# Kernel optimization log

Measured on AMD Instinct MI355X. Metric: run time of the kernel, lower is better.

The kernel has to match this reference:

```python
import jax, jax.numpy as jnp
import numpy as np


def setup_inputs() -> dict:
    key = jax.random.key(0)
    k1, k2 = jax.random.split(key)
    x = jax.random.normal(k1, (4, 2048, 2048), dtype=jnp.float32)
    weight = jax.random.normal(k2, (8192, 2048), dtype=jnp.float32) * 0.02
    return {"x": x, "weight": weight, "bits": 8}


def reference(x, weight, bits):
    # ---- activation quantization (per-row int8-style) ----
    scale = jnp.clip(jnp.max(jnp.abs(x), axis=-1, keepdims=True), 1e-5)  # [..., 1]
    max_val = (1 << (bits - 1)) - 1  # 127 for 8 bits
    x_q = jnp.clip(jnp.round(x * (max_val / scale)), -max_val, max_val)

    # ---- ternary weight quantization (-1, 0, 1) ----
    w_scale = jnp.mean(jnp.abs(weight))
    w_q = jnp.where(weight > 0.5 * w_scale, 1.0, 0.0) + jnp.where(
        weight < -0.5 * w_scale, -1.0, 0.0
    )

    # ---- dequantized linear: (x_q @ (w_q * w_scale)^T) / x_scale ----
    out = jnp.einsum("bsi,oi->bso", x_q, w_q * w_scale) / scale

    # ---- squared ReLU ----
    return jnp.maximum(out, 0.0) ** 2
```

## Files before the change

### kernel.cpp

```cpp
#include <hip/hip_runtime.h>
#include <hip/hip_bf16.h>

typedef __attribute__((ext_vector_type(4))) int i32x4;
typedef __attribute__((ext_vector_type(16))) int i32x16;

#define M_DIM 8192
#define N_DIM 8192
#define K_DIM 2048
#define WCOUNT (N_DIM * K_DIM)


__global__ __launch_bounds__(256) void k_abs_partial(const float* __restrict__ w,
                                                     float* __restrict__ part) {
    int tid = blockIdx.x * 256 + threadIdx.x;
    const float4* w4 = (const float4*)w;
    float s = 0.0f;
    const int total4 = WCOUNT / 4;
    for (int i = tid; i < total4; i += 2048 * 256) {
        float4 v = w4[i];
        s += fabsf(v.x) + fabsf(v.y) + fabsf(v.z) + fabsf(v.w);
    }
    #pragma unroll
    for (int off = 1; off < 64; off <<= 1) s += __shfl_xor(s, off);
    __shared__ float red[4];
    if ((threadIdx.x & 63) == 0) red[threadIdx.x >> 6] = s;
    __syncthreads();
    if (threadIdx.x == 0)
        part[blockIdx.x] = (red[0] + red[1]) + (red[2] + red[3]);
}

__global__ __launch_bounds__(256) void k_abs_final(const float* __restrict__ part,
                                                   float* __restrict__ sum) {
    int t = threadIdx.x;
    float s = 0.0f;
    #pragma unroll
    for (int i = 0; i < 8; i++) s += part[t + i * 256];
    #pragma unroll
    for (int off = 1; off < 64; off <<= 1) s += __shfl_xor(s, off);
    __shared__ float red[4];
    if ((t & 63) == 0) red[t >> 6] = s;
    __syncthreads();
    if (t == 0) sum[0] = (red[0] + red[1]) + (red[2] + red[3]);
}

__global__ __launch_bounds__(256) void k_wquant(const float* __restrict__ w,
                                                const float* __restrict__ sum,
                                                signed char* __restrict__ wqf) {
    const float thr = 0.5f * (sum[0] * (1.0f / 16777216.0f));
    const int g = blockIdx.x * 256 + threadIdx.x;
    const int n = g >> 7;
    const int kc = g & 127;
    const float4* wr = (const float4*)(w + (size_t)n * K_DIM + kc * 16);
    union { signed char c[16]; uint4 v; } pk;
    #pragma unroll
    for (int q = 0; q < 4; q++) {
        float4 v = wr[q];
        pk.c[q * 4 + 0] = v.x > thr ? 1 : (v.x < -thr ? -1 : 0);
        pk.c[q * 4 + 1] = v.y > thr ? 1 : (v.y < -thr ? -1 : 0);
        pk.c[q * 4 + 2] = v.z > thr ? 1 : (v.z < -thr ? -1 : 0);
        pk.c[q * 4 + 3] = v.w > thr ? 1 : (v.w < -thr ? -1 : 0);
    }
    *(uint4*)(wqf + (size_t)(n >> 5) * 65536 + kc * 512 + (n & 31) * 16) = pk.v;
}

__global__ __launch_bounds__(256) void k_xquant(const float* __restrict__ x,
                                                const float* __restrict__ sum,
                                                signed char* __restrict__ xqf,
                                                float* __restrict__ coef) {
    const int row = blockIdx.x;
    const int t = threadIdx.x;
    const float4* xr = (const float4*)(x + (size_t)row * K_DIM);
    float4 a = xr[t * 2];
    float4 b = xr[t * 2 + 1];
    float m = fmaxf(fmaxf(fmaxf(fabsf(a.x), fabsf(a.y)), fmaxf(fabsf(a.z), fabsf(a.w))),
                    fmaxf(fmaxf(fabsf(b.x), fabsf(b.y)), fmaxf(fabsf(b.z), fabsf(b.w))));
    #pragma unroll
    for (int off = 1; off < 64; off <<= 1) m = fmaxf(m, __shfl_xor(m, off));
    __shared__ float red[4];
    if ((t & 63) == 0) red[t >> 6] = m;
    __syncthreads();
    m = fmaxf(fmaxf(red[0], red[1]), fmaxf(red[2], red[3]));
    const float sc = fmaxf(m, 1e-5f);
    if (t == 0) coef[row] = (sum[0] * (1.0f / 16777216.0f)) / sc;
    const float r = 127.0f / sc;
    float q[8] = {a.x, a.y, a.z, a.w, b.x, b.y, b.z, b.w};
    union { signed char c[8]; uint2 v; } pk;
    #pragma unroll
    for (int j = 0; j < 8; j++) {
        float v = rintf(q[j] * r);
        v = fminf(fmaxf(v, -127.0f), 127.0f);
        pk.c[j] = (signed char)v;
    }
    *(uint2*)(xqf + (size_t)(row >> 5) * 65536 + (t >> 1) * 512
              + (row & 31) * 16 + (t & 1) * 8) = pk.v;
}

#define GLDS16(g, l)                                                                   \
    __builtin_amdgcn_global_load_lds((const __attribute__((address_space(1))) void*)(g), \
                                     (__attribute__((address_space(3))) void*)(l), 16, 0, 0)
#define BAR __builtin_amdgcn_s_barrier()
#define VMW(n) asm volatile("s_waitcnt vmcnt(" #n ")" ::: "memory")

__global__ __launch_bounds__(256, 4) void k_gemm(const signed char* __restrict__ xqf,
                                                 const signed char* __restrict__ wqf,
                                                 const float* __restrict__ coef,
                                                 float* __restrict__ out) {
    __shared__ signed char lds[32768];

    const int t = threadIdx.x;
    const int lane = t & 63;
    const int wid = t >> 6;
    const int wm = wid >> 1;
    const int wn = wid & 1;
    const int l31 = lane & 31;
    const int kg = lane >> 5;

    const int bid = blockIdx.x;
    const int xcd = bid & 7;
    const int idx = bid >> 3;
    const int grp = idx >> 5;
    const int w_ = idx & 31;
    const int bcol = grp * 4 + (w_ & 3);
    const int brow = xcd * 8 + ((w_ >> 2) & 7);

    const signed char* aSrc0 = xqf + (size_t)(brow * 4 + (t >> 7)) * 65536 + (t & 127) * 16;
    const signed char* aSrc1 = xqf + (size_t)(brow * 4 + 2 + (t >> 7)) * 65536 + (t & 127) * 16;
    const signed char* bSrc0 = wqf + (size_t)(bcol * 4 + (t >> 7)) * 65536 + (t & 127) * 16;
    const signed char* bSrc1 = wqf + (size_t)(bcol * 4 + 2 + (t >> 7)) * 65536 + (t & 127) * 16;
    const int dst0 = wid * 1024;
    const int dst1 = 4096 + wid * 1024;

#define STG(bufc, kt) do {                                                         \
        GLDS16(aSrc0 + (size_t)(kt) * 2048, lds + (bufc) * 16384 + dst0);          \
        GLDS16(aSrc1 + (size_t)(kt) * 2048, lds + (bufc) * 16384 + dst1);          \
        GLDS16(bSrc0 + (size_t)(kt) * 2048, lds + (bufc) * 16384 + 8192 + dst0);   \
        GLDS16(bSrc1 + (size_t)(kt) * 2048, lds + (bufc) * 16384 + 8192 + dst1);   \
    } while (0)

    const int aRd = wm * 4096 + lane * 16;
    const int bRd = 8192 + wn * 4096 + lane * 16;

    i32x16 acc00 = (i32x16){0,0,0,0,0,0,0,0,0,0,0,0,0,0,0,0};
    i32x16 acc01 = acc00, acc10 = acc00, acc11 = acc00;

#define MMK(bufc) do {                                                             \
        const int ab = (bufc) * 16384 + aRd;                                       \
        const int bb = (bufc) * 16384 + bRd;                                       \
        i32x4 a00 = *(const i32x4*)&lds[ab];                                       \
        i32x4 a10 = *(const i32x4*)&lds[ab + 2048];                                \
        i32x4 b00 = *(const i32x4*)&lds[bb];                                       \
        i32x4 b10 = *(const i32x4*)&lds[bb + 2048];                                \
        i32x4 a01 = *(const i32x4*)&lds[ab + 1024];                                \
        i32x4 a11 = *(const i32x4*)&lds[ab + 3072];                                \
        i32x4 b01 = *(const i32x4*)&lds[bb + 1024];                                \
        i32x4 b11 = *(const i32x4*)&lds[bb + 3072];                                \
        __builtin_amdgcn_s_setprio(1);                                             \
        acc00 = __builtin_amdgcn_mfma_i32_32x32x32_i8(a00, b00, acc00, 0, 0, 0);   \
        acc01 = __builtin_amdgcn_mfma_i32_32x32x32_i8(a00, b10, acc01, 0, 0, 0);   \
        acc10 = __builtin_amdgcn_mfma_i32_32x32x32_i8(a10, b00, acc10, 0, 0, 0);   \
        acc11 = __builtin_amdgcn_mfma_i32_32x32x32_i8(a10, b10, acc11, 0, 0, 0);   \
        acc00 = __builtin_amdgcn_mfma_i32_32x32x32_i8(a01, b01, acc00, 0, 0, 0);   \
        acc01 = __builtin_amdgcn_mfma_i32_32x32x32_i8(a01, b11, acc01, 0, 0, 0);   \
        acc10 = __builtin_amdgcn_mfma_i32_32x32x32_i8(a11, b01, acc10, 0, 0, 0);   \
        acc11 = __builtin_amdgcn_mfma_i32_32x32x32_i8(a11, b11, acc11, 0, 0, 0);   \
        __builtin_amdgcn_s_setprio(0); } while (0)

    STG(0, 0);
    STG(1, 1);
    VMW(4);
    BAR;

    #pragma unroll 1
    for (int j = 0; j < 15; j++) {
        const int kt = 2 * j;
        MMK(0); BAR;
        STG(0, kt + 2); VMW(4);
        BAR;
        MMK(1); BAR;
        STG(1, kt + 3); VMW(4);
        BAR;
    }
    MMK(0); BAR;
    VMW(0);
    BAR;
    MMK(1);

    const int rb = brow * 128 + wm * 64 + 4 * kg;
    const int cb = bcol * 128 + wn * 64 + l31;
    #pragma unroll
    for (int mt = 0; mt < 2; mt++) {
        const i32x16 ac0 = mt ? acc10 : acc00;
        const i32x16 ac1 = mt ? acc11 : acc01;
        #pragma unroll
        for (int r = 0; r < 16; r++) {
            const int grow = rb + mt * 32 + (r & 3) + 8 * (r >> 2);
            const float c = coef[grow];
            float v0 = (float)ac0[r] * c; v0 = fmaxf(v0, 0.0f);
            float v1 = (float)ac1[r] * c; v1 = fmaxf(v1, 0.0f);
            __builtin_nontemporal_store(v0 * v0, &out[(size_t)grow * N_DIM + cb]);
            __builtin_nontemporal_store(v1 * v1, &out[(size_t)grow * N_DIM + cb + 32]);
        }
    }
#undef STG
#undef MMK
}

extern "C" void kernel_launch(void* const* d_in, const int* in_sizes, int n_in,
                              void* d_out, int out_size, void* d_ws, size_t ws_size,
                              hipStream_t stream) {
    const float* x = (const float*)d_in[0];
    const float* w = (const float*)d_in[1];
    float* out = (float*)d_out;

    char* ws = (char*)d_ws;
    float* sum   = (float*)ws;
    float* part  = (float*)(ws + 256);
    float* coef  = (float*)(ws + 49152);
    signed char* xqf = (signed char*)(ws + 131072);
    signed char* wqf = (signed char*)(ws + 131072 + 16777216);

    k_abs_partial<<<2048, 256, 0, stream>>>(w, part);
    k_abs_final<<<1, 256, 0, stream>>>(part, sum);
    k_wquant<<<4096, 256, 0, stream>>>(w, sum, wqf);
    k_xquant<<<M_DIM, 256, 0, stream>>>(x, sum, xqf, coef);
    k_gemm<<<dim3(4096), 256, 0, stream>>>(xqf, wqf, coef, out);
}
```

Before: 194.4 us.

## Drop LDS staging in int8 GEMM and load MFMA fragments directly from global

The GEMM stops staging A/B tiles through LDS with global_load_lds and barriers. Each wave now loads its MFMA fragments straight from the pre-swizzled global buffers into registers, double-buffered in registers (fx/fy), and occupancy is lowered to 3 blocks per SM. This removes LDS traffic and barrier sync. The cost is that tiles shared between waves (each A tile is used by two waves, likewise each B tile) are fetched twice from L2/global, and register pressure goes up.

```diff
diff --git a/kernel.cpp b/kernel.cpp
--- a/kernel.cpp
+++ b/kernel.cpp
@@ -95,18 +95,10 @@
               + (row & 31) * 16 + (t & 1) * 8) = pk.v;
 }
 
-#define GLDS16(g, l)                                                                   \
-    __builtin_amdgcn_global_load_lds((const __attribute__((address_space(1))) void*)(g), \
-                                     (__attribute__((address_space(3))) void*)(l), 16, 0, 0)
-#define BAR __builtin_amdgcn_s_barrier()
-#define VMW(n) asm volatile("s_waitcnt vmcnt(" #n ")" ::: "memory")
-
-__global__ __launch_bounds__(256, 4) void k_gemm(const signed char* __restrict__ xqf,
+__global__ __launch_bounds__(256, 3) void k_gemm(const signed char* __restrict__ xqf,
                                                  const signed char* __restrict__ wqf,
                                                  const float* __restrict__ coef,
                                                  float* __restrict__ out) {
-    __shared__ signed char lds[32768];
-
     const int t = threadIdx.x;
     const int lane = t & 63;
     const int wid = t >> 6;
@@ -123,74 +115,55 @@
     const int bcol = grp * 4 + (w_ & 3);
     const int brow = xcd * 8 + ((w_ >> 2) & 7);
 
-    const signed char* aSrc0 = xqf + (size_t)(brow * 4 + (t >> 7)) * 65536 + (t & 127) * 16;
-    const signed char* aSrc1 = xqf + (size_t)(brow * 4 + 2 + (t >> 7)) * 65536 + (t & 127) * 16;
-    const signed char* bSrc0 = wqf + (size_t)(bcol * 4 + (t >> 7)) * 65536 + (t & 127) * 16;
-    const signed char* bSrc1 = wqf + (size_t)(bcol * 4 + 2 + (t >> 7)) * 65536 + (t & 127) * 16;
-    const int dst0 = wid * 1024;
-    const int dst1 = 4096 + wid * 1024;
-
-#define STG(bufc, kt) do {                                                         \
-        GLDS16(aSrc0 + (size_t)(kt) * 2048, lds + (bufc) * 16384 + dst0);          \
-        GLDS16(aSrc1 + (size_t)(kt) * 2048, lds + (bufc) * 16384 + dst1);          \
-        GLDS16(bSrc0 + (size_t)(kt) * 2048, lds + (bufc) * 16384 + 8192 + dst0);   \
-        GLDS16(bSrc1 + (size_t)(kt) * 2048, lds + (bufc) * 16384 + 8192 + dst1);   \
-    } while (0)
-
-    const int aRd = wm * 4096 + lane * 16;
-    const int bRd = 8192 + wn * 4096 + lane * 16;
-
-    i32x16 acc00 = (i32x16){0,0,0,0,0,0,0,0,0,0,0,0,0,0,0,0};
-    i32x16 acc01 = acc00, acc10 = acc00, acc11 = acc00;
-
-#define MMK(bufc) do {                                                             \
-        const int ab = (bufc) * 16384 + aRd;                                       \
-        const int bb = (bufc) * 16384 + bRd;                                       \
-        i32x4 a00 = *(const i32x4*)&lds[ab];                                       \
-        i32x4 a10 = *(const i32x4*)&lds[ab + 2048];                                \
-        i32x4 b00 = *(const i32x4*)&lds[bb];                                       \
-        i32x4 b10 = *(const i32x4*)&lds[bb + 2048];                                \
-        i32x4 a01 = *(const i32x4*)&lds[ab + 1024];                                \
-        i32x4 a11 = *(const i32x4*)&lds[ab + 3072];                                \
-        i32x4 b01 = *(const i32x4*)&lds[bb + 1024];                                \
-        i32x4 b11 = *(const i32x4*)&lds[bb + 3072];                                \
+    const signed char* pa0 = xqf + (size_t)(brow * 4 + wm * 2) * 65536 + lane * 16;
+    const signed char* pa1 = pa0 + 65536;
+    const signed char* pb0 = wqf + (size_t)(bcol * 4 + wn * 2) * 65536 + lane * 16;
+    const signed char* pb1 = pb0 + 65536;
+
+    i32x16 c00 = (i32x16){0,0,0,0,0,0,0,0,0,0,0,0,0,0,0,0};
+    i32x16 c01 = c00, c10 = c00, c11 = c00;
+    i32x4 fx[8], fy[8];
+
+#define LOADF(F, o) do {                                                           \
+        F[0] = *(const i32x4*)(pa0 + (o));                                         \
+        F[1] = *(const i32x4*)(pa0 + (o) + 1024);                                  \
+        F[2] = *(const i32x4*)(pa1 + (o));                                         \
+        F[3] = *(const i32x4*)(pa1 + (o) + 1024);                                  \
+        F[4] = *(const i32x4*)(pb0 + (o));                                         \
+        F[5] = *(const i32x4*)(pb0 + (o) + 1024);                                  \
+        F[6] = *(const i32x4*)(pb1 + (o));                                         \
+        F[7] = *(const i32x4*)(pb1 + (o) + 1024); } while (0)
+#define MMF(F) do {                                                                \
         __builtin_amdgcn_s_setprio(1);                                             \
-        acc00 = __builtin_amdgcn_mfma_i32_32x32x32_i8(a00, b00, acc00, 0, 0, 0);   \
-        acc01 = __builtin_amdgcn_mfma_i32_32x32x32_i8(a00, b10, acc01, 0, 0, 0);   \
-        acc10 = __builtin_amdgcn_mfma_i32_32x32x32_i8(a10, b00, acc10, 0, 0, 0);   \
-        acc11 = __builtin_amdgcn_mfma_i32_32x32x32_i8(a10, b10, acc11, 0, 0, 0);   \
-        acc00 = __builtin_amdgcn_mfma_i32_32x32x32_i8(a01, b01, acc00, 0, 0, 0);   \
-        acc01 = __builtin_amdgcn_mfma_i32_32x32x32_i8(a01, b11, acc01, 0, 0, 0);   \
-        acc10 = __builtin_amdgcn_mfma_i32_32x32x32_i8(a11, b01, acc10, 0, 0, 0);   \
-        acc11 = __builtin_amdgcn_mfma_i32_32x32x32_i8(a11, b11, acc11, 0, 0, 0);   \
+        c00 = __builtin_amdgcn_mfma_i32_32x32x32_i8(F[0], F[4], c00, 0, 0, 0);     \
+        c01 = __builtin_amdgcn_mfma_i32_32x32x32_i8(F[0], F[6], c01, 0, 0, 0);     \
+        c10 = __builtin_amdgcn_mfma_i32_32x32x32_i8(F[2], F[4], c10, 0, 0, 0);     \
+        c11 = __builtin_amdgcn_mfma_i32_32x32x32_i8(F[2], F[6], c11, 0, 0, 0);     \
+        c00 = __builtin_amdgcn_mfma_i32_32x32x32_i8(F[1], F[5], c00, 0, 0, 0);     \
+        c01 = __builtin_amdgcn_mfma_i32_32x32x32_i8(F[1], F[7], c01, 0, 0, 0);     \
+        c10 = __builtin_amdgcn_mfma_i32_32x32x32_i8(F[3], F[5], c10, 0, 0, 0);     \
+        c11 = __builtin_amdgcn_mfma_i32_32x32x32_i8(F[3], F[7], c11, 0, 0, 0);     \
         __builtin_amdgcn_s_setprio(0); } while (0)
 
-    STG(0, 0);
-    STG(1, 1);
-    VMW(4);
-    BAR;
-
+    LOADF(fx, 0);
     #pragma unroll 1
     for (int j = 0; j < 15; j++) {
-        const int kt = 2 * j;
-        MMK(0); BAR;
-        STG(0, kt + 2); VMW(4);
-        BAR;
-        MMK(1); BAR;
-        STG(1, kt + 3); VMW(4);
-        BAR;
-    }
-    MMK(0); BAR;
-    VMW(0);
-    BAR;
-    MMK(1);
+        LOADF(fy, 2048);
+        MMF(fx);
+        pa0 += 4096; pa1 += 4096; pb0 += 4096; pb1 += 4096;
+        LOADF(fx, 0);
+        MMF(fy);
+    }
+    LOADF(fy, 2048);
+    MMF(fx);
+    MMF(fy);
 
     const int rb = brow * 128 + wm * 64 + 4 * kg;
     const int cb = bcol * 128 + wn * 64 + l31;
     #pragma unroll
     for (int mt = 0; mt < 2; mt++) {
-        const i32x16 ac0 = mt ? acc10 : acc00;
-        const i32x16 ac1 = mt ? acc11 : acc01;
+        const i32x16 ac0 = mt ? c10 : c00;
+        const i32x16 ac1 = mt ? c11 : c01;
         #pragma unroll
         for (int r = 0; r < 16; r++) {
             const int grow = rb + mt * 32 + (r & 3) + 8 * (r >> 2);
@@ -201,8 +174,8 @@
             __builtin_nontemporal_store(v1 * v1, &out[(size_t)grow * N_DIM + cb + 32]);
         }
     }
-#undef STG
-#undef MMK
+#undef LOADF
+#undef MMF
 }
 
 extern "C" void kernel_launch(void* const* d_in, const int* in_sizes, int n_in,
```

New measurement: 253.1 us. 1.3x slower.
